# Optimization experiments

Measured on AMD Instinct MI355X. Metric: run time of the kernel, lower is better.

The kernel has to match this reference:

```python
import jax, jax.numpy as jnp
import numpy as np

H = 16
D = 1024
DK = D // H


def setup_inputs() -> dict:
    key = jax.random.key(0)
    ks = jax.random.split(key, 10)
    B, S = 2, 2048
    scale = 1.0 / np.sqrt(D)
    inp = {
        "query": jax.random.normal(ks[0], (B, S, D), jnp.float32),
        "key_": jax.random.normal(ks[1], (B, S, D), jnp.float32),
        "value": jax.random.normal(ks[2], (B, S, D), jnp.float32),
        "Wq": jax.random.normal(ks[3], (D, D), jnp.float32) * scale,
        "bq": jnp.zeros((D,), jnp.float32),
        "Wk": jax.random.normal(ks[4], (D, D), jnp.float32) * scale,
        "bk": jnp.zeros((D,), jnp.float32),
        "Wv": jax.random.normal(ks[5], (D, D), jnp.float32) * scale,
        "bv": jnp.zeros((D,), jnp.float32),
        "ln_gamma": jnp.ones((D,), jnp.float32),
        "ln_beta": jnp.zeros((D,), jnp.float32),
    }
    return inp


def reference(query, key_, value, Wq, bq, Wk, bk, Wv, bv, ln_gamma, ln_beta):
    B, S, _ = query.shape
    residual = query
    # projections, split into heads: [B, H, S, DK]
    def proj(x, W, b):
        return (x @ W + b).reshape(B, -1, H, DK).transpose(0, 2, 1, 3)
    q = proj(query, Wq, bq)
    k = proj(key_, Wk, bk)
    v = proj(value, Wv, bv)
    # scaled dot-product attention with full score matrix (as in source)
    scores = jnp.einsum("bhqd,bhkd->bhqk", q, k) / jnp.sqrt(jnp.float32(DK))
    p_att = jax.nn.softmax(scores, axis=-1)  # dropout p=0 -> identity
    x = jnp.einsum("bhqk,bhkd->bhqd", p_att, v)
    x = x.transpose(0, 2, 1, 3).reshape(B, S, D)
    # residual + LayerNorm(eps=1e-6)
    y = x + residual
    mu = jnp.mean(y, axis=-1, keepdims=True)
    var = jnp.var(y, axis=-1, keepdims=True)
    y = (y - mu) / jnp.sqrt(var + 1e-6)
    return y * ln_gamma + ln_beta
```

## Files before the change

### kernel.cpp

```cpp
#include <hip/hip_runtime.h>


typedef float f32x4 __attribute__((ext_vector_type(4)));
typedef short short8 __attribute__((ext_vector_type(8)));
typedef unsigned int uint32x2 __attribute__((ext_vector_type(2)));

__device__ __forceinline__ unsigned short f2bf(float f) {
    unsigned u = __builtin_bit_cast(unsigned, f);
    u += 0x7fffu + ((u >> 16) & 1u);
    return (unsigned short)(u >> 16);
}
__device__ __forceinline__ unsigned packbf2(float lo, float hi) {
    return __builtin_amdgcn_perm(__builtin_bit_cast(unsigned, hi),
                                 __builtin_bit_cast(unsigned, lo), 0x07060302u);
}

__device__ __forceinline__ void g2l16(const unsigned short* g, unsigned short* l) {
    __builtin_amdgcn_global_load_lds(
        (const __attribute__((address_space(1))) unsigned int*)g,
        (__attribute__((address_space(3))) unsigned int*)l, 16, 0, 0);
}

__global__ __launch_bounds__(256) void convert_all(
    const float* __restrict__ xq, const float* __restrict__ xk, const float* __restrict__ xv,
    const float* __restrict__ Wq, const float* __restrict__ Wk, const float* __restrict__ Wv,
    unsigned short* __restrict__ xout, unsigned short* __restrict__ wout)
{
    const int bx  = blockIdx.x;
    const int tid = threadIdx.x;
    if (bx < 6144) {
        const int z = bx >> 11;
        const float* src = (z == 0) ? xq : (z == 1) ? xk : xv;
        const size_t idx = ((size_t)(bx & 2047) * 256 + tid) * 8;
        const float4 a = *(const float4*)(src + idx);
        const float4 b = *(const float4*)(src + idx + 4);
        short8 o;
        o[0] = (short)f2bf(a.x); o[1] = (short)f2bf(a.y);
        o[2] = (short)f2bf(a.z); o[3] = (short)f2bf(a.w);
        o[4] = (short)f2bf(b.x); o[5] = (short)f2bf(b.y);
        o[6] = (short)f2bf(b.z); o[7] = (short)f2bf(b.w);
        *(short8*)(xout + (size_t)z * 4194304 + idx) = o;
    } else {
        const int i = bx - 6144;
        const int z = i >> 8, tile = i & 255;
        const float* W = (z == 0) ? Wq : (z == 1) ? Wk : Wv;
        unsigned short* Wt = wout + (size_t)z * 1048576;
        __shared__ unsigned short Ts[64 * 65];
        const int kb0 = (tile >> 4) * 64, nb0 = (tile & 15) * 64;
        const int a = tid >> 6, b = tid & 63;
#pragma unroll
        for (int j = 0; j < 16; ++j) {
            const int k = j * 4 + a, n = b;
            Ts[n * 65 + k] = f2bf(W[(size_t)(kb0 + k) * 1024 + nb0 + n]);
        }
        __syncthreads();
#pragma unroll
        for (int j = 0; j < 16; ++j) {
            const int n = j * 4 + a, k = b;
            Wt[(size_t)(nb0 + n) * 1024 + kb0 + k] = Ts[n * 65 + k];
        }
    }
}

__global__ __launch_bounds__(256) void qkv_gemm(
    const unsigned short* __restrict__ Xb, const unsigned short* __restrict__ Wtb,
    const float* __restrict__ bq, const float* __restrict__ bk, const float* __restrict__ bv,
    unsigned short* __restrict__ qo, unsigned short* __restrict__ ko, unsigned short* __restrict__ vo)
{
    const int z = blockIdx.z;
    const unsigned short* X  = Xb  + (size_t)z * 4194304;
    const unsigned short* Wt = Wtb + (size_t)z * 1048576;
    const float* bias   = (z == 0) ? bq : (z == 1) ? bk : bv;
    unsigned short* out = (z == 0) ? qo : (z == 1) ? ko : vo;

    __shared__ unsigned short smem[16384];

    const int tid  = threadIdx.x;
    const int wave = tid >> 6;
    const int lane = tid & 63;
    const int l15  = lane & 15;
    const int quad = lane >> 4;
    const int mq   = wave & 1, nq = wave >> 1;
    const int mbase = blockIdx.x * 128, nbase = blockIdx.y * 128;

    const int srow = lane >> 2;
    const int schk = (lane & 3) ^ (srow & 3);

    const unsigned short* srcA = X  + (size_t)(mbase + wave * 32 + srow) * 1024 + schk * 8;
    const unsigned short* srcB = Wt + (size_t)(nbase + wave * 32 + srow) * 1024 + schk * 8;

    f32x4 acc[4][4];
#pragma unroll
    for (int i = 0; i < 4; ++i)
#pragma unroll
        for (int j = 0; j < 4; ++j) acc[i][j] = (f32x4){0.f, 0.f, 0.f, 0.f};

#pragma unroll
    for (int t = 0; t < 2; ++t) {
        g2l16(srcA + (size_t)t * 16 * 1024, &smem[(wave * 32 + t * 16) * 32]);
        g2l16(srcB + (size_t)t * 16 * 1024, &smem[4096 + (wave * 32 + t * 16) * 32]);
    }

    for (int it = 0; it < 32; ++it) {
        const int boff = (it & 1) * 8192;
        __syncthreads();

        if (it + 1 < 32) {
            const int poff = boff ^ 8192;
            const size_t ko2 = (size_t)(it + 1) * 32;
#pragma unroll
            for (int t = 0; t < 2; ++t) {
                g2l16(srcA + (size_t)t * 16 * 1024 + ko2, &smem[poff + (wave * 32 + t * 16) * 32]);
                g2l16(srcB + (size_t)t * 16 * 1024 + ko2, &smem[poff + 4096 + (wave * 32 + t * 16) * 32]);
            }
        }

        short8 af[4], bf[4];
#pragma unroll
        for (int i = 0; i < 4; ++i) {
            af[i] = *(const short8*)(&smem[boff + (mq * 64 + i * 16 + l15) * 32 + ((quad ^ (l15 & 3)) << 3)]);
            bf[i] = *(const short8*)(&smem[boff + 4096 + (nq * 64 + i * 16 + l15) * 32 + ((quad ^ (l15 & 3)) << 3)]);
        }
#pragma unroll
        for (int mt = 0; mt < 4; ++mt)
#pragma unroll
            for (int nt = 0; nt < 4; ++nt)
                acc[mt][nt] = __builtin_amdgcn_mfma_f32_16x16x32_bf16(af[mt], bf[nt], acc[mt][nt], 0, 0, 0);
    }

    __syncthreads();

    float bvals[4];
#pragma unroll
    for (int nt = 0; nt < 4; ++nt) bvals[nt] = bias[nbase + nq * 64 + nt * 16 + l15];

    if (z == 2) {
        unsigned short* Epv = smem;
        const int hbase = nbase >> 6;
        const int b     = mbase >> 11;
        const int srow0 = mbase & 2047;
#pragma unroll
        for (int nt = 0; nt < 4; ++nt) {
            __syncthreads();
            short8 w[2];
#pragma unroll
            for (int e = 0; e < 2; ++e)
#pragma unroll
                for (int j = 0; j < 8; ++j) {
                    const int idx = e * 8 + j, mt2 = idx & 3, r = idx >> 2;
                    w[e][j] = (short)f2bf(acc[mt2][nt][r] + bvals[nt]);
                }
            unsigned short* dst = &Epv[(nq * 16 + l15) * 136 + mq * 64 + quad * 16];
            *(short8*)(dst)     = w[0];
            *(short8*)(dst + 8) = w[1];
            __syncthreads();
            const int row = tid >> 3;
            const int d   = nt * 16 + (row & 15);
            const int h   = hbase + (row >> 4);
#pragma unroll
            for (int e = 0; e < 2; ++e) {
                const int colb = e * 64 + (tid & 7) * 8;
                short8 v = *(const short8*)(&Epv[row * 136 + colb]);
                *(short8*)(&out[((size_t)(b * 16 + h) * 64 + d) * 2048 + srow0 + colb]) = v;
            }
        }
    } else {
        unsigned short* Ep = smem + wave * 1152;
        const int hQ = (nbase + nq * 64) >> 6;
        const float scl = (z == 0) ? 0.18033688f : 1.0f;
#pragma unroll
        for (int mt = 0; mt < 4; ++mt) {
#pragma unroll
            for (int nt = 0; nt < 4; ++nt)
#pragma unroll
                for (int r = 0; r < 4; ++r)
                    Ep[(quad * 4 + r) * 72 + nt * 16 + l15] =
                        f2bf((acc[mt][nt][r] + bvals[nt]) * scl);
#pragma unroll
            for (int half = 0; half < 2; ++half) {
                const int m = (lane >> 3) + half * 8;
                const int nblk = lane & 7;
                short8 v = *(const short8*)(&Ep[m * 72 + nblk * 8]);
                const int gm = mbase + mq * 64 + mt * 16 + m;
                const int b2 = gm >> 11, srw = gm & 2047;
                *(short8*)(&out[((size_t)(b2 * 16 + hQ) * 2048 + srw) * 64 + nblk * 8]) = v;
            }
        }
    }
}

__global__ __launch_bounds__(256) void attn(
    const unsigned short* __restrict__ qb, const unsigned short* __restrict__ kb,
    const unsigned short* __restrict__ vtb, float* __restrict__ xw)
{
    const int tid  = threadIdx.x;
    const int wave = tid >> 6;
    const int lane = tid & 63;
    const int l15  = lane & 15;
    const int quad = lane >> 4;

    const int bh    = blockIdx.x;
    const int qbase = blockIdx.y * 128 + wave * 32;

    __shared__ unsigned short Ks[2][64 * 64];
    __shared__ unsigned short Vs[2][64 * 64];
    __shared__ unsigned short Pt[4][2][16][72];

    short8 qf[2][2];
#pragma unroll
    for (int mt = 0; mt < 2; ++mt) {
        const unsigned short* Qp = qb + ((size_t)bh * 2048 + qbase + mt * 16 + l15) * 64 + quad * 8;
        qf[mt][0] = *(const short8*)(Qp);
        qf[mt][1] = *(const short8*)(Qp + 32);
    }

    const unsigned short* Kbh = kb  + (size_t)bh * 2048 * 64;
    const unsigned short* Vbh = vtb + (size_t)bh * 64 * 2048;

    const int r8 = lane >> 3, c8 = lane & 7;
    const unsigned short *srcK[2], *srcV[2];
#pragma unroll
    for (int t = 0; t < 2; ++t) {
        const int row = wave * 16 + t * 8 + r8;
        srcK[t] = Kbh + (size_t)row * 64   + ((c8 ^ r8) << 3);
        srcV[t] = Vbh + (size_t)row * 2048 + ((c8 ^ r8) << 3);
    }

    float l_r[2][4] = {{0.f,0.f,0.f,0.f},{0.f,0.f,0.f,0.f}};
    f32x4 O[2][4];
#pragma unroll
    for (int mt = 0; mt < 2; ++mt)
#pragma unroll
        for (int i = 0; i < 4; ++i) O[mt][i] = (f32x4){0.f, 0.f, 0.f, 0.f};

#pragma unroll
    for (int t = 0; t < 2; ++t) {
        g2l16(srcK[t], &Ks[0][(wave * 16 + t * 8) * 64]);
        g2l16(srcV[t], &Vs[0][(wave * 16 + t * 8) * 64]);
    }

    for (int it = 0; it < 32; ++it) {
        const int buf = it & 1;
        __syncthreads();

        if (it + 1 < 32) {
            const size_t kn = (size_t)(it + 1) * 64;
#pragma unroll
            for (int t = 0; t < 2; ++t) {
                g2l16(srcK[t] + kn * 64, &Ks[buf ^ 1][(wave * 16 + t * 8) * 64]);
                g2l16(srcV[t] + kn,      &Vs[buf ^ 1][(wave * 16 + t * 8) * 64]);
            }
        }

        short8 kf[4][2];
#pragma unroll
        for (int ct = 0; ct < 4; ++ct)
#pragma unroll
            for (int kk = 0; kk < 2; ++kk)
                kf[ct][kk] = *(const short8*)(&Ks[buf][(ct * 16 + l15) * 64 +
                                                  ((((kk << 2) + quad) ^ (l15 & 7)) << 3)]);

#pragma unroll
        for (int mt = 0; mt < 2; ++mt) {
            f32x4 sc[4];
#pragma unroll
            for (int ct = 0; ct < 4; ++ct) {
                f32x4 a = {0.f, 0.f, 0.f, 0.f};
                a = __builtin_amdgcn_mfma_f32_16x16x32_bf16(qf[mt][0], kf[ct][0], a, 0, 0, 0);
                a = __builtin_amdgcn_mfma_f32_16x16x32_bf16(qf[mt][1], kf[ct][1], a, 0, 0, 0);
                sc[ct] = a;
            }
#pragma unroll
            for (int r = 0; r < 4; ++r) {
                const float p0 = __builtin_amdgcn_exp2f(sc[0][r]);
                const float p1 = __builtin_amdgcn_exp2f(sc[1][r]);
                const float p2 = __builtin_amdgcn_exp2f(sc[2][r]);
                const float p3 = __builtin_amdgcn_exp2f(sc[3][r]);
                l_r[mt][r] += (p0 + p1) + (p2 + p3);
                uint32x2 pk = {packbf2(p0, p1), packbf2(p2, p3)};
                *(uint32x2*)(&Pt[wave][mt][quad * 4 + r][l15 * 4]) = pk;
            }
        }

#pragma unroll
        for (int c = 0; c < 2; ++c) {
            const short8 pf0 = *(const short8*)(&Pt[wave][0][l15][c * 32 + quad * 8]);
            const short8 pf1 = *(const short8*)(&Pt[wave][1][l15][c * 32 + quad * 8]);
#pragma unroll
            for (int ct4 = 0; ct4 < 4; ++ct4) {
                const short8 vf = *(const short8*)(&Vs[buf][(ct4 * 16 + l15) * 64 +
                                                       ((((c << 2) + quad) ^ (l15 & 7)) << 3)]);
                O[0][ct4] = __builtin_amdgcn_mfma_f32_16x16x32_bf16(pf0, vf, O[0][ct4], 0, 0, 0);
                O[1][ct4] = __builtin_amdgcn_mfma_f32_16x16x32_bf16(pf1, vf, O[1][ct4], 0, 0, 0);
            }
        }
    }

    float inv[2][4];
#pragma unroll
    for (int mt = 0; mt < 2; ++mt)
#pragma unroll
        for (int r = 0; r < 4; ++r) {
            float s = l_r[mt][r];
#pragma unroll
            for (int off = 8; off >= 1; off >>= 1) s += __shfl_xor(s, off);
            inv[mt][r] = 1.0f / s;
        }

    const int b = bh >> 4, h = bh & 15;
#pragma unroll
    for (int mt = 0; mt < 2; ++mt)
#pragma unroll
        for (int ct4 = 0; ct4 < 4; ++ct4)
#pragma unroll
            for (int r = 0; r < 4; ++r) {
                const int s = qbase + mt * 16 + quad * 4 + r;
                xw[((size_t)b * 2048 + s) * 1024 + h * 64 + ct4 * 16 + l15] =
                    O[mt][ct4][r] * inv[mt][r];
            }
}

__global__ __launch_bounds__(256) void ln_kernel(
    const float* __restrict__ xw, const float* __restrict__ res,
    const float* __restrict__ gamma, const float* __restrict__ beta,
    float* __restrict__ out)
{
    const int row = blockIdx.x;
    const int tid = threadIdx.x;
    const size_t base = (size_t)row * 1024 + tid * 4;

    const float4 x  = *(const float4*)(xw + base);
    const float4 rv = *(const float4*)(res + base);
    float4 y;
    y.x = x.x + rv.x; y.y = x.y + rv.y; y.z = x.z + rv.z; y.w = x.w + rv.w;

    float s  = y.x + y.y + y.z + y.w;
    float s2 = y.x * y.x + y.y * y.y + y.z * y.z + y.w * y.w;
#pragma unroll
    for (int off = 32; off >= 1; off >>= 1) {
        s  += __shfl_xor(s, off);
        s2 += __shfl_xor(s2, off);
    }
    __shared__ float red[8];
    const int wave = tid >> 6;
    if ((tid & 63) == 0) { red[wave] = s; red[4 + wave] = s2; }
    __syncthreads();
    s  = red[0] + red[1] + red[2] + red[3];
    s2 = red[4] + red[5] + red[6] + red[7];

    const float mu   = s * (1.0f / 1024.0f);
    const float var  = s2 * (1.0f / 1024.0f) - mu * mu;
    const float rstd = rsqrtf(var + 1e-6f);

    const float4 g  = *(const float4*)(gamma + tid * 4);
    const float4 bt = *(const float4*)(beta + tid * 4);
    float4 o;
    o.x = (y.x - mu) * rstd * g.x + bt.x;
    o.y = (y.y - mu) * rstd * g.y + bt.y;
    o.z = (y.z - mu) * rstd * g.z + bt.z;
    o.w = (y.w - mu) * rstd * g.w + bt.w;
    *(float4*)(out + base) = o;
}

extern "C" void kernel_launch(void* const* d_in, const int* in_sizes, int n_in,
                              void* d_out, int out_size, void* d_ws, size_t ws_size,
                              hipStream_t stream) {
    const float* query = (const float*)d_in[0];
    const float* key_  = (const float*)d_in[1];
    const float* value = (const float*)d_in[2];
    const float* Wq    = (const float*)d_in[3];
    const float* bq    = (const float*)d_in[4];
    const float* Wk    = (const float*)d_in[5];
    const float* bk    = (const float*)d_in[6];
    const float* Wv    = (const float*)d_in[7];
    const float* bv    = (const float*)d_in[8];
    const float* ln_g  = (const float*)d_in[9];
    const float* ln_b  = (const float*)d_in[10];
    float* out = (float*)d_out;

    const size_t MB = 1024 * 1024;
    char* ws = (char*)d_ws;
    unsigned short* Xbuf = (unsigned short*)(ws);
    float*          xwp  = (float*)(ws);
    unsigned short* Wtb  = (unsigned short*)(ws + 24 * MB);
    unsigned short* qbuf = (unsigned short*)(ws + 30 * MB);
    unsigned short* kbuf = (unsigned short*)(ws + 38 * MB);
    unsigned short* vtb  = (unsigned short*)(ws + 46 * MB);

    convert_all<<<6912,           256, 0, stream>>>(query, key_, value, Wq, Wk, Wv, Xbuf, Wtb);
    qkv_gemm   <<<dim3(32, 8, 3), 256, 0, stream>>>(Xbuf, Wtb, bq, bk, bv, qbuf, kbuf, vtb);
    attn       <<<dim3(32, 16),   256, 0, stream>>>(qbuf, kbuf, vtb, xwp);
    ln_kernel  <<<4096,           256, 0, stream>>>(xwp, query, ln_g, ln_b, out);
}
```

Baseline: 211.2 us.

## Transpose attention MFMAs so P stays in registers, drop LDS round-trip

```diff
diff --git a/kernel.cpp b/kernel.cpp
--- a/kernel.cpp
+++ b/kernel.cpp
@@ -3,7 +3,7 @@
 
 typedef float f32x4 __attribute__((ext_vector_type(4)));
 typedef short short8 __attribute__((ext_vector_type(8)));
-typedef unsigned int uint32x2 __attribute__((ext_vector_type(2)));
+typedef unsigned int uint32x4 __attribute__((ext_vector_type(4)));
 
 __device__ __forceinline__ unsigned short f2bf(float f) {
     unsigned u = __builtin_bit_cast(unsigned, f);
@@ -147,12 +147,12 @@
             for (int e = 0; e < 2; ++e)
 #pragma unroll
                 for (int j = 0; j < 8; ++j) {
-                    const int idx = e * 8 + j, mt2 = idx & 3, r = idx >> 2;
+                    const int mt2 = 2 * e + (j >> 2), r = j & 3;
                     w[e][j] = (short)f2bf(acc[mt2][nt][r] + bvals[nt]);
                 }
-            unsigned short* dst = &Epv[(nq * 16 + l15) * 136 + mq * 64 + quad * 16];
-            *(short8*)(dst)     = w[0];
-            *(short8*)(dst + 8) = w[1];
+            unsigned short* dst = &Epv[(nq * 16 + l15) * 136 + mq * 64 + quad * 8];
+            *(short8*)(dst)      = w[0];
+            *(short8*)(dst + 32) = w[1];
             __syncthreads();
             const int row = tid >> 3;
             const int d   = nt * 16 + (row & 15);
@@ -204,14 +204,14 @@
 
     __shared__ unsigned short Ks[2][64 * 64];
     __shared__ unsigned short Vs[2][64 * 64];
-    __shared__ unsigned short Pt[4][2][16][72];
+    __shared__ float Ow[4][32 * 68];
 
     short8 qf[2][2];
 #pragma unroll
-    for (int mt = 0; mt < 2; ++mt) {
-        const unsigned short* Qp = qb + ((size_t)bh * 2048 + qbase + mt * 16 + l15) * 64 + quad * 8;
-        qf[mt][0] = *(const short8*)(Qp);
-        qf[mt][1] = *(const short8*)(Qp + 32);
+    for (int nt = 0; nt < 2; ++nt) {
+        const unsigned short* Qp = qb + ((size_t)bh * 2048 + qbase + nt * 16 + l15) * 64 + quad * 8;
+        qf[nt][0] = *(const short8*)(Qp);
+        qf[nt][1] = *(const short8*)(Qp + 32);
     }
 
     const unsigned short* Kbh = kb  + (size_t)bh * 2048 * 64;
@@ -226,12 +226,12 @@
         srcV[t] = Vbh + (size_t)row * 2048 + ((c8 ^ r8) << 3);
     }
 
-    float l_r[2][4] = {{0.f,0.f,0.f,0.f},{0.f,0.f,0.f,0.f}};
+    float l_part[2] = {0.f, 0.f};
     f32x4 O[2][4];
 #pragma unroll
-    for (int mt = 0; mt < 2; ++mt)
-#pragma unroll
-        for (int i = 0; i < 4; ++i) O[mt][i] = (f32x4){0.f, 0.f, 0.f, 0.f};
+    for (int nt = 0; nt < 2; ++nt)
+#pragma unroll
+        for (int i = 0; i < 4; ++i) O[nt][i] = (f32x4){0.f, 0.f, 0.f, 0.f};
 
 #pragma unroll
     for (int t = 0; t < 2; ++t) {
@@ -254,70 +254,80 @@
 
         short8 kf[4][2];
 #pragma unroll
-        for (int ct = 0; ct < 4; ++ct)
-#pragma unroll
-            for (int kk = 0; kk < 2; ++kk)
-                kf[ct][kk] = *(const short8*)(&Ks[buf][(ct * 16 + l15) * 64 +
-                                                  ((((kk << 2) + quad) ^ (l15 & 7)) << 3)]);
-
-#pragma unroll
-        for (int mt = 0; mt < 2; ++mt) {
-            f32x4 sc[4];
-#pragma unroll
-            for (int ct = 0; ct < 4; ++ct) {
+        for (int mt = 0; mt < 4; ++mt)
+#pragma unroll
+            for (int dc = 0; dc < 2; ++dc)
+                kf[mt][dc] = *(const short8*)(&Ks[buf][(mt * 16 + l15) * 64 +
+                                                  ((((dc << 2) + quad) ^ (l15 & 7)) << 3)]);
+
+        f32x4 sc[4][2];
+#pragma unroll
+        for (int mt = 0; mt < 4; ++mt)
+#pragma unroll
+            for (int nt = 0; nt < 2; ++nt) {
                 f32x4 a = {0.f, 0.f, 0.f, 0.f};
-                a = __builtin_amdgcn_mfma_f32_16x16x32_bf16(qf[mt][0], kf[ct][0], a, 0, 0, 0);
-                a = __builtin_amdgcn_mfma_f32_16x16x32_bf16(qf[mt][1], kf[ct][1], a, 0, 0, 0);
-                sc[ct] = a;
-            }
-#pragma unroll
-            for (int r = 0; r < 4; ++r) {
-                const float p0 = __builtin_amdgcn_exp2f(sc[0][r]);
-                const float p1 = __builtin_amdgcn_exp2f(sc[1][r]);
-                const float p2 = __builtin_amdgcn_exp2f(sc[2][r]);
-                const float p3 = __builtin_amdgcn_exp2f(sc[3][r]);
-                l_r[mt][r] += (p0 + p1) + (p2 + p3);
-                uint32x2 pk = {packbf2(p0, p1), packbf2(p2, p3)};
-                *(uint32x2*)(&Pt[wave][mt][quad * 4 + r][l15 * 4]) = pk;
-            }
-        }
+                a = __builtin_amdgcn_mfma_f32_16x16x32_bf16(kf[mt][0], qf[nt][0], a, 0, 0, 0);
+                a = __builtin_amdgcn_mfma_f32_16x16x32_bf16(kf[mt][1], qf[nt][1], a, 0, 0, 0);
+                sc[mt][nt] = a;
+            }
+
+#pragma unroll
+        for (int mt = 0; mt < 4; ++mt)
+#pragma unroll
+            for (int nt = 0; nt < 2; ++nt) {
+#pragma unroll
+                for (int r = 0; r < 4; ++r) {
+                    const float p = __builtin_amdgcn_exp2f(sc[mt][nt][r]);
+                    sc[mt][nt][r] = p;
+                    l_part[nt] += p;
+                }
+            }
 
 #pragma unroll
         for (int c = 0; c < 2; ++c) {
-            const short8 pf0 = *(const short8*)(&Pt[wave][0][l15][c * 32 + quad * 8]);
-            const short8 pf1 = *(const short8*)(&Pt[wave][1][l15][c * 32 + quad * 8]);
-#pragma unroll
-            for (int ct4 = 0; ct4 < 4; ++ct4) {
-                const short8 vf = *(const short8*)(&Vs[buf][(ct4 * 16 + l15) * 64 +
+            short8 pf[2];
+#pragma unroll
+            for (int nt = 0; nt < 2; ++nt) {
+                uint32x4 pu;
+                pu[0] = packbf2(sc[2 * c][nt][0],     sc[2 * c][nt][1]);
+                pu[1] = packbf2(sc[2 * c][nt][2],     sc[2 * c][nt][3]);
+                pu[2] = packbf2(sc[2 * c + 1][nt][0], sc[2 * c + 1][nt][1]);
+                pu[3] = packbf2(sc[2 * c + 1][nt][2], sc[2 * c + 1][nt][3]);
+                pf[nt] = __builtin_bit_cast(short8, pu);
+            }
+#pragma unroll
+            for (int dt = 0; dt < 4; ++dt) {
+                const short8 vf = *(const short8*)(&Vs[buf][(dt * 16 + l15) * 64 +
                                                        ((((c << 2) + quad) ^ (l15 & 7)) << 3)]);
-                O[0][ct4] = __builtin_amdgcn_mfma_f32_16x16x32_bf16(pf0, vf, O[0][ct4], 0, 0, 0);
-                O[1][ct4] = __builtin_amdgcn_mfma_f32_16x16x32_bf16(pf1, vf, O[1][ct4], 0, 0, 0);
-            }
-        }
-    }
-
-    float inv[2][4];
-#pragma unroll
-    for (int mt = 0; mt < 2; ++mt)
-#pragma unroll
-        for (int r = 0; r < 4; ++r) {
-            float s = l_r[mt][r];
-#pragma unroll
-            for (int off = 8; off >= 1; off >>= 1) s += __shfl_xor(s, off);
-            inv[mt][r] = 1.0f / s;
+                O[0][dt] = __builtin_amdgcn_mfma_f32_16x16x32_bf16(vf, pf[0], O[0][dt], 0, 0, 0);
+                O[1][dt] = __builtin_amdgcn_mfma_f32_16x16x32_bf16(vf, pf[1], O[1][dt], 0, 0, 0);
+            }
+        }
+    }
+
+    float inv[2];
+#pragma unroll
+    for (int nt = 0; nt < 2; ++nt) {
+        float s = l_part[nt];
+        s += __shfl_xor(s, 16);
+        s += __shfl_xor(s, 32);
+        inv[nt] = 1.0f / s;
+    }
+
+#pragma unroll
+    for (int nt = 0; nt < 2; ++nt)
+#pragma unroll
+        for (int dt = 0; dt < 4; ++dt) {
+            f32x4 v = O[nt][dt];
+            v[0] *= inv[nt]; v[1] *= inv[nt]; v[2] *= inv[nt]; v[3] *= inv[nt];
+            *(f32x4*)(&Ow[wave][(nt * 16 + l15) * 68 + dt * 16 + quad * 4]) = v;
         }
 
     const int b = bh >> 4, h = bh & 15;
-#pragma unroll
-    for (int mt = 0; mt < 2; ++mt)
-#pragma unroll
-        for (int ct4 = 0; ct4 < 4; ++ct4)
-#pragma unroll
-            for (int r = 0; r < 4; ++r) {
-                const int s = qbase + mt * 16 + quad * 4 + r;
-                xw[((size_t)b * 2048 + s) * 1024 + h * 64 + ct4 * 16 + l15] =
-                    O[mt][ct4][r] * inv[mt][r];
-            }
+    const size_t obase = ((size_t)b * 2048 + qbase) * 1024 + h * 64 + lane;
+#pragma unroll
+    for (int qq = 0; qq < 32; ++qq)
+        xw[obase + (size_t)qq * 1024] = Ow[wave][qq * 68 + lane];
 }
 
 __global__ __launch_bounds__(256) void ln_kernel(
```

New measurement: 207.9 us. Within noise of the previous version (-1.6%).
